# Kernel tuning notes

Hardware: AMD Instinct MI355X
Metric: run time of the kernel (lower is better)

## Reference

```python
import jax, jax.numpy as jnp
import numpy as np

B, SEQ, D = 2, 1024, 768
E, H = 8, 3072          # num_experts, expert hidden (mlp_ratio=4)
CAPACITY = 2            # k = CAPACITY * num_tokens


def setup_inputs() -> dict:
    key = jax.random.key(0)
    ks = jax.random.split(key, 6)
    x = jax.random.normal(ks[0], (B, SEQ, D), dtype=jnp.float32)
    gate_weight = jax.random.normal(ks[1], (E, D), dtype=jnp.float32) * 0.006
    w1 = jax.random.normal(ks[2], (E, D, H), dtype=jnp.float32) * (1.0 / np.sqrt(D))
    b1 = jnp.zeros((E, H), dtype=jnp.float32)
    w2 = jax.random.normal(ks[3], (E, H, D), dtype=jnp.float32) * (1.0 / np.sqrt(H))
    b2 = jnp.zeros((E, D), dtype=jnp.float32)
    return {"x": x, "gate_weight": gate_weight, "w1": w1, "b1": b1, "w2": w2, "b2": b2}


def reference(x, gate_weight, w1, b1, w2, b2):
    Bb, s, d = x.shape
    xf = x.reshape(-1, d)                     # [S, D]
    S = xf.shape[0]
    k = S * CAPACITY
    logits = xf @ gate_weight.T               # [S, E]
    scores = jax.nn.softmax(logits, axis=-1).T  # [E, S]
    # flattened top-k over all (expert, token) pairs -> sparse gate matrix
    vals, idx = jax.lax.top_k(scores.reshape(-1), k)
    gate = jnp.zeros((E * S,), dtype=x.dtype).at[idx].add(vals).reshape(E, S)
    # expert MLPs (GELU-tanh) applied per expert; zero gate entries kill
    # non-routed (expert, token) pairs -> same math as gather/MLP/scatter.
    h = jax.nn.gelu(jnp.einsum('sd,edh->esh', xf, w1) + b1[:, None, :], approximate=True)
    out = jnp.einsum('esh,ehd->esd', h, w2) + b2[:, None, :]   # [E, S, D]
    y = jnp.einsum('es,esd->sd', gate, out)    # weighted combine + sum over experts
    return y.reshape(Bb, s, d)
```

## Files before the change

kernel.cpp:

```cpp
#include <hip/hip_runtime.h>
#include <math.h>

#define S_TOK 2048
#define NEXP  8
#define DDIM  768
#define HDIM  3072
#define KSEL  4096

typedef __attribute__((ext_vector_type(8))) short short8;
typedef __attribute__((ext_vector_type(4))) float f32x4;
typedef __attribute__((ext_vector_type(2))) unsigned int u32x2;

__device__ __forceinline__ unsigned short f2bf(float f) {
  unsigned u = __float_as_uint(f);
  u += 0x7fffu + ((u >> 16) & 1u);
  return (unsigned short)(u >> 16);
}

__device__ __forceinline__ float gelu_fast(float v) {
  float u = 0.7978845608028654f * (v + 0.044715f * v * v * v);
  float t = __expf(-2.0f * fabsf(u));
  float th = (1.0f - t) / (1.0f + t);
  th = copysignf(th, u);
  return 0.5f * v * (1.0f + th);
}

__global__ __launch_bounds__(256) void zero_kernel(float* __restrict__ p, int n) {
  int i = blockIdx.x * 256 + threadIdx.x;
  if (i < n) p[i] = 0.f;
}

__global__ __launch_bounds__(256) void convx_kernel(const float* __restrict__ x,
                                                    short* __restrict__ xb) {
  int i = (blockIdx.x * 256 + threadIdx.x) * 8;
  float4 a = *(const float4*)(x + i);
  float4 b = *(const float4*)(x + i + 4);
  short8 v;
  v[0] = (short)f2bf(a.x); v[1] = (short)f2bf(a.y);
  v[2] = (short)f2bf(a.z); v[3] = (short)f2bf(a.w);
  v[4] = (short)f2bf(b.x); v[5] = (short)f2bf(b.y);
  v[6] = (short)f2bf(b.z); v[7] = (short)f2bf(b.w);
  *(short8*)(xb + i) = v;
}

__global__ __launch_bounds__(256) void gate_kernel(
    const float* __restrict__ x, const float* __restrict__ gw,
    float* __restrict__ scores)
{
  int tid  = threadIdx.x;
  int lane = tid & 63;
  int wid  = tid >> 6;
  int token = blockIdx.x * 4 + wid;
  const float* xr = x + (size_t)token * DDIM;

  float acc[NEXP];
#pragma unroll
  for (int e = 0; e < NEXP; ++e) acc[e] = 0.f;

  for (int d = lane; d < DDIM; d += 64) {
    float xv = xr[d];
#pragma unroll
    for (int e = 0; e < NEXP; ++e) acc[e] += xv * gw[e * DDIM + d];
  }
#pragma unroll
  for (int e = 0; e < NEXP; ++e) {
    for (int off = 32; off; off >>= 1) acc[e] += __shfl_down(acc[e], off, 64);
  }
  if (lane == 0) {
    float m = acc[0];
#pragma unroll
    for (int e = 1; e < NEXP; ++e) m = fmaxf(m, acc[e]);
    float p[NEXP], s = 0.f;
#pragma unroll
    for (int e = 0; e < NEXP; ++e) { p[e] = expf(acc[e] - m); s += p[e]; }
    float inv = 1.0f / s;
#pragma unroll
    for (int e = 0; e < NEXP; ++e) scores[e * S_TOK + token] = p[e] * inv;
  }
}

__device__ unsigned block_scan_excl(unsigned v, volatile unsigned* wsum) {
  int tid = threadIdx.x, lane = tid & 63, wid = tid >> 6;
  __syncthreads();
  unsigned x = v;
#pragma unroll
  for (int off = 1; off < 64; off <<= 1) {
    unsigned t = __shfl_up(x, off, 64);
    if (lane >= off) x += t;
  }
  if (lane == 63) wsum[wid] = x;
  __syncthreads();
  if (tid < 64) {
    unsigned w = (lane < 16) ? wsum[lane] : 0u;
#pragma unroll
    for (int off = 1; off < 16; off <<= 1) {
      unsigned t = __shfl_up(w, off, 64);
      if (lane >= off) w += t;
    }
    if (lane < 16) wsum[lane] = w;
  }
  __syncthreads();
  unsigned woff = (wid > 0) ? wsum[wid - 1] : 0u;
  return woff + (x - v);
}

__global__ __launch_bounds__(1024) void select_kernel(
    const float* __restrict__ scores,
    int* __restrict__ tokenlist, float* __restrict__ slotgate,
    int* __restrict__ offsets)
{
  __shared__ unsigned cnt;
  __shared__ unsigned wsum[16];
  int tid = threadIdx.x;
  int base = tid * 16;

  float sv[16]; unsigned key[16];
#pragma unroll
  for (int j = 0; j < 16; ++j) {
    sv[j] = scores[base + j];
    key[j] = __float_as_uint(sv[j]);
  }

  unsigned lo = 0, hi = 0x3F800000u;
  while (lo < hi) {
    unsigned mid = lo + ((hi - lo + 1) >> 1);
    if (tid == 0) cnt = 0;
    __syncthreads();
    unsigned c = 0;
#pragma unroll
    for (int j = 0; j < 16; ++j) c += (key[j] >= mid) ? 1u : 0u;
    for (int off = 32; off; off >>= 1) c += __shfl_down(c, off, 64);
    if ((tid & 63) == 0) atomicAdd(&cnt, c);
    __syncthreads();
    unsigned tot = cnt;
    __syncthreads();
    if (tot >= (unsigned)KSEL) lo = mid; else hi = mid - 1;
  }
  unsigned V = lo;

  if (tid == 0) cnt = 0;
  __syncthreads();
  {
    unsigned c = 0;
#pragma unroll
    for (int j = 0; j < 16; ++j) c += (key[j] > V) ? 1u : 0u;
    for (int off = 32; off; off >>= 1) c += __shfl_down(c, off, 64);
    if ((tid & 63) == 0) atomicAdd(&cnt, c);
  }
  __syncthreads();
  int need = KSEL - (int)cnt;
  __syncthreads();

  unsigned tloc = 0;
#pragma unroll
  for (int j = 0; j < 16; ++j) tloc += (key[j] == V) ? 1u : 0u;
  unsigned texcl = block_scan_excl(tloc, wsum);

  unsigned selmask = 0, sloc = 0, trun = texcl;
#pragma unroll
  for (int j = 0; j < 16; ++j) {
    bool f;
    if (key[j] > V) f = true;
    else if (key[j] == V) { f = ((int)trun < need); ++trun; }
    else f = false;
    if (f) { selmask |= (1u << j); ++sloc; }
  }
  unsigned sexcl = block_scan_excl(sloc, wsum);

  if ((tid & 127) == 0) offsets[tid >> 7] = (int)sexcl;
  if (tid == 0) offsets[NEXP] = KSEL;

  unsigned p = sexcl;
#pragma unroll
  for (int j = 0; j < 16; ++j) {
    int i = base + j;
    if (selmask & (1u << j)) {
      tokenlist[p] = i & (S_TOK - 1);
      slotgate[p] = sv[j];
      ++p;
    }
  }
}

template <int MODE>
__global__ __launch_bounds__(128) void moe_mfma(
    const short* __restrict__ Abase, const float* __restrict__ W,
    const float* __restrict__ bias, void* __restrict__ outp,
    const int* __restrict__ offsets, const int* __restrict__ tokenlist,
    const float* __restrict__ slotgate)
{
  const int e = (int)blockIdx.x;
  const int K = (MODE == 1) ? DDIM : HDIM;
  const int N = (MODE == 1) ? HDIM : DDIM;
  const int tile  = (MODE == 1) ? (int)blockIdx.z : ((int)blockIdx.z >> 2);
  const int split = (MODE == 1) ? 0 : ((int)blockIdx.z & 3);
  const int klen  = 768;
  const int kb = split * klen;

  const int r0 = offsets[e];
  const int rows = offsets[e + 1] - r0;
  const int rowbase = tile << 7;
  if (rowbase >= rows) return;
  int vr = rows - rowbase; if (vr > 128) vr = 128;
  const int colbase = (int)blockIdx.y << 6;

  __shared__ short As[128 * 40];
  __shared__ __align__(16) short Bs[32 * 64];
  const unsigned bs_lds = (unsigned)(uintptr_t)&Bs[0];

  const int tid = threadIdx.x;
  const int lane = tid & 63;
  const int wid = tid >> 6;
  const int wr = wid << 6;
  const int l15 = lane & 15;
  const int lq = lane >> 4;

  const short* arow;
  {
    int cr = (tid < vr) ? tid : (vr - 1);
    if (MODE == 1) arow = Abase + (size_t)tokenlist[r0 + rowbase + cr] * DDIM;
    else           arow = Abase + (size_t)(r0 + rowbase + cr) * HDIM + kb;
  }

  const int brow = tid >> 2;
  const int bc4 = tid & 3;
  const float* wsrc = W + (size_t)e * K * N + (size_t)kb * N + colbase + bc4 * 4;
  const int bwbase = ((tid >> 4) << 9) + ((brow & 3) << 5) + (bc4 << 3);

  f32x4 acc[4][4];
#pragma unroll
  for (int i = 0; i < 4; ++i)
#pragma unroll
    for (int j = 0; j < 4; ++j) acc[i][j] = (f32x4){0.f, 0.f, 0.f, 0.f};

  short8 av[4];
  float4 bw[4];

#define LOAD_AB(KN)                                              \
  {                                                              \
    _Pragma("unroll")                                            \
    for (int m = 0; m < 4; ++m)                                  \
      av[m] = *(const short8*)(arow + (KN) + m * 8);             \
    const float* wp = wsrc + (size_t)((KN) + brow) * N;          \
    _Pragma("unroll")                                            \
    for (int q = 0; q < 4; ++q) bw[q] = *(const float4*)(wp + q * 16); \
  }

#define WRITE_LDS()                                              \
  {                                                              \
    _Pragma("unroll")                                            \
    for (int m = 0; m < 4; ++m)                                  \
      *(short8*)&As[tid * 40 + m * 8] = av[m];                   \
    _Pragma("unroll")                                            \
    for (int q = 0; q < 4; ++q) {                                \
      u32x2 pk;                                                  \
      pk[0] = (unsigned)f2bf(bw[q].x) | ((unsigned)f2bf(bw[q].y) << 16); \
      pk[1] = (unsigned)f2bf(bw[q].z) | ((unsigned)f2bf(bw[q].w) << 16); \
      *(u32x2*)((char*)Bs + bwbase + (q << 7)) = pk;             \
    }                                                            \
  }

  LOAD_AB(0);

#pragma unroll 1
  for (int k0 = 0; k0 < klen; k0 += 32) {
    __syncthreads();
    WRITE_LDS();
    __syncthreads();
    if (k0 + 32 < klen) LOAD_AB(k0 + 32);
    short8 af[4], bfr[4];
#pragma unroll
    for (int i = 0; i < 4; ++i)
      af[i] = *(const short8*)&As[(wr + i * 16 + l15) * 40 + lq * 8];
#pragma unroll
    for (int j = 0; j < 4; ++j) {
      unsigned off = bs_lds + ((unsigned)(8 * lq + j) << 7) + ((unsigned)l15 << 3);
      union { short8 s; u32x2 u[2]; } fb;
      asm volatile("ds_read_b64_tr_b16 %0, %2 offset:0\n\t"
                   "ds_read_b64_tr_b16 %1, %2 offset:512"
                   : "=&v"(fb.u[0]), "=&v"(fb.u[1]) : "v"(off));
      bfr[j] = fb.s;
    }
    asm volatile("s_waitcnt lgkmcnt(0)" ::: "memory");
    __builtin_amdgcn_sched_barrier(0);
#pragma unroll
    for (int i = 0; i < 4; ++i)
#pragma unroll
      for (int j = 0; j < 4; ++j)
        acc[i][j] = __builtin_amdgcn_mfma_f32_16x16x32_bf16(af[i], bfr[j], acc[i][j], 0, 0, 0);
  }

  if (MODE == 1) {
    short* hb = (short*)outp;
    const float* bp = bias + (size_t)e * N + colbase;
#pragma unroll
    for (int i = 0; i < 4; ++i) {
      int rb = wr + i * 16 + lq * 4;
#pragma unroll
      for (int j = 0; j < 4; ++j) {
        int col = j * 16 + l15;
        float bvv = bp[col];
#pragma unroll
        for (int p = 0; p < 4; ++p) {
          int r = rb + p;
          if (r < vr)
            hb[(size_t)(r0 + rowbase + r) * HDIM + colbase + col] =
                (short)f2bf(gelu_fast(acc[i][j][p] + bvv));
        }
      }
    }
  } else {
    float* y = (float*)outp;
    const float* bp = bias + (size_t)e * N + colbase;
#pragma unroll
    for (int i = 0; i < 4; ++i) {
      int rb = wr + i * 16 + lq * 4;
#pragma unroll
      for (int p = 0; p < 4; ++p) {
        int r = rb + p;
        if (r < vr) {
          int gi = r0 + rowbase + r;
          float g = slotgate[gi];
          float* yrow = y + (size_t)tokenlist[gi] * N + colbase;
#pragma unroll
          for (int j = 0; j < 4; ++j) {
            int col = j * 16 + l15;
            float v = acc[i][j][p] + (split == 0 ? bp[col] : 0.f);
            atomicAdd(&yrow[col], g * v);
          }
        }
      }
    }
  }
}

extern "C" void kernel_launch(void* const* d_in, const int* in_sizes, int n_in,
                              void* d_out, int out_size, void* d_ws, size_t ws_size,
                              hipStream_t stream) {
  const float* x  = (const float*)d_in[0];
  const float* gw = (const float*)d_in[1];
  const float* w1 = (const float*)d_in[2];
  const float* b1 = (const float*)d_in[3];
  const float* w2 = (const float*)d_in[4];
  const float* b2 = (const float*)d_in[5];
  float* y = (float*)d_out;

  char* ws = (char*)d_ws;
  float* scores    = (float*)(ws);
  int*   tokenlist = (int*)(ws + (64 << 10));
  float* slotgate  = (float*)(ws + (80 << 10));
  int*   offsets   = (int*)(ws + (96 << 10));
  short* xbf       = (short*)(ws + (128 << 10));
  short* hbuf      = (short*)(ws + (128 << 10) + (size_t)S_TOK * DDIM * 2);

  zero_kernel<<<(out_size + 255) / 256, 256, 0, stream>>>(y, out_size);
  convx_kernel<<<S_TOK * DDIM / 2048, 256, 0, stream>>>(x, xbf);
  gate_kernel<<<S_TOK / 4, 256, 0, stream>>>(x, gw, scores);
  select_kernel<<<1, 1024, 0, stream>>>(scores, tokenlist, slotgate, offsets);

  dim3 g1(NEXP, HDIM / 64, 16);
  moe_mfma<1><<<g1, 128, 0, stream>>>(xbf, w1, b1, hbuf, offsets, tokenlist, slotgate);
  dim3 g2(NEXP, DDIM / 64, 64);
  moe_mfma<2><<<g2, 128, 0, stream>>>(hbuf, w2, b2, y, offsets, tokenlist, slotgate);
}
```

Before: 238.4 us.

## Pre-convert expert weights to bf16 and stage tiles via direct global-to-LDS loads

Adds a conversion kernel that writes W1 and W2 to bf16 in the workspace, chunked along the hidden dimension when the workspace is too small. The MFMA kernels then read bf16 weights with global_load_lds straight into LDS instead of loading fp32 into registers, converting and storing. The tile grows to 128x128 with 256 threads and four waves in a 2x2 layout. This removes the in-loop conversion and register staging and halves weight bytes in the GEMM loop, at the cost of extra full-weight conversion passes (read fp32, write bf16) on every call.

```diff
diff --git a/kernel.cpp b/kernel.cpp
--- a/kernel.cpp
+++ b/kernel.cpp
@@ -10,6 +10,11 @@
 typedef __attribute__((ext_vector_type(8))) short short8;
 typedef __attribute__((ext_vector_type(4))) float f32x4;
 typedef __attribute__((ext_vector_type(2))) unsigned int u32x2;
+
+#define GLOAD_LDS(GP, LP)                                            \
+  __builtin_amdgcn_global_load_lds(                                  \
+      (__attribute__((address_space(1))) void*)(GP),                 \
+      (__attribute__((address_space(3))) void*)(LP), 16, 0, 0)
 
 __device__ __forceinline__ unsigned short f2bf(float f) {
   unsigned u = __float_as_uint(f);
@@ -43,6 +48,26 @@
   *(short8*)(xb + i) = v;
 }
 
+__global__ __launch_bounds__(256) void convw_kernel(
+    const float* __restrict__ src, short* __restrict__ dst,
+    int ncols_src, int col0, int ncols_dst, int row0, int nrows, int nrows_src)
+{
+  long long i = ((long long)blockIdx.x * 256 + threadIdx.x) * 8;
+  int n = (int)(i % ncols_dst);
+  long long rr = i / ncols_dst;
+  int r = (int)(rr % nrows);
+  int e = (int)(rr / nrows);
+  const float* s = src + ((size_t)e * nrows_src + row0 + r) * ncols_src + col0 + n;
+  float4 a = *(const float4*)(s);
+  float4 b = *(const float4*)(s + 4);
+  short8 v;
+  v[0] = (short)f2bf(a.x); v[1] = (short)f2bf(a.y);
+  v[2] = (short)f2bf(a.z); v[3] = (short)f2bf(a.w);
+  v[4] = (short)f2bf(b.x); v[5] = (short)f2bf(b.y);
+  v[6] = (short)f2bf(b.z); v[7] = (short)f2bf(b.w);
+  *(short8*)(dst + i) = v;
+}
+
 __global__ __launch_bounds__(256) void gate_kernel(
     const float* __restrict__ x, const float* __restrict__ gw,
     float* __restrict__ scores)
@@ -183,49 +208,66 @@
 }
 
 template <int MODE>
-__global__ __launch_bounds__(128) void moe_mfma(
-    const short* __restrict__ Abase, const float* __restrict__ W,
+__global__ __launch_bounds__(256) void moe_mfma(
+    const short* __restrict__ Abase, const short* __restrict__ Wbf,
     const float* __restrict__ bias, void* __restrict__ outp,
     const int* __restrict__ offsets, const int* __restrict__ tokenlist,
-    const float* __restrict__ slotgate)
+    const float* __restrict__ slotgate,
+    int N, int SA, int estride, int split_bits, int cbias, int bias_en)
 {
   const int e = (int)blockIdx.x;
-  const int K = (MODE == 1) ? DDIM : HDIM;
-  const int N = (MODE == 1) ? HDIM : DDIM;
-  const int tile  = (MODE == 1) ? (int)blockIdx.z : ((int)blockIdx.z >> 2);
-  const int split = (MODE == 1) ? 0 : ((int)blockIdx.z & 3);
-  const int klen  = 768;
-  const int kb = split * klen;
+  const int tile  = (int)blockIdx.z >> split_bits;
+  const int split = (int)blockIdx.z & ((1 << split_bits) - 1);
+  const int kb = split * 768;
 
   const int r0 = offsets[e];
   const int rows = offsets[e + 1] - r0;
   const int rowbase = tile << 7;
   if (rowbase >= rows) return;
   int vr = rows - rowbase; if (vr > 128) vr = 128;
-  const int colbase = (int)blockIdx.y << 6;
-
-  __shared__ short As[128 * 40];
-  __shared__ __align__(16) short Bs[32 * 64];
+  const int colbase = (int)blockIdx.y << 7;
+
+  __shared__ __align__(16) short As[128 * 32];
+  __shared__ __align__(16) short Bs[64 * 64];
   const unsigned bs_lds = (unsigned)(uintptr_t)&Bs[0];
 
   const int tid = threadIdx.x;
   const int lane = tid & 63;
   const int wid = tid >> 6;
-  const int wr = wid << 6;
+  const int wr = (wid >> 1) << 6;
+  const int wc = (wid & 1) << 6;
   const int l15 = lane & 15;
   const int lq = lane >> 4;
 
-  const short* arow;
-  {
-    int cr = (tid < vr) ? tid : (vr - 1);
-    if (MODE == 1) arow = Abase + (size_t)tokenlist[r0 + rowbase + cr] * DDIM;
-    else           arow = Abase + (size_t)(r0 + rowbase + cr) * HDIM + kb;
-  }
-
-  const int brow = tid >> 2;
-  const int bc4 = tid & 3;
-  const float* wsrc = W + (size_t)e * K * N + (size_t)kb * N + colbase + bc4 * 4;
-  const int bwbase = ((tid >> 4) << 9) + ((brow & 3) << 5) + (bc4 << 3);
+  const int row0 = (wid * 2) * 16 + (lane >> 2);
+  const int row1 = row0 + 16;
+  const int cr0 = (row0 < vr) ? row0 : (vr - 1);
+  const int cr1 = (row1 < vr) ? row1 : (vr - 1);
+  const short *aptr0, *aptr1;
+  if (MODE == 1) {
+    aptr0 = Abase + (size_t)tokenlist[r0 + rowbase + cr0] * SA + ((lane & 3) << 3);
+    aptr1 = Abase + (size_t)tokenlist[r0 + rowbase + cr1] * SA + ((lane & 3) << 3);
+  } else {
+    aptr0 = Abase + (size_t)(r0 + rowbase + cr0) * SA + kb + ((lane & 3) << 3);
+    aptr1 = Abase + (size_t)(r0 + rowbase + cr1) * SA + kb + ((lane & 3) << 3);
+  }
+
+  const short* wb = Wbf + (size_t)e * estride + colbase +
+                    ((lane >> 3) << 4) + ((lane & 1) << 3) +
+                    (size_t)(kb + ((lane & 7) >> 1)) * N;
+  const short* bptr0 = wb + (size_t)(wid * 2 + 0) * 4 * N;
+  const short* bptr1 = wb + (size_t)(wid * 2 + 1) * 4 * N;
+
+  const int dst0 = wid * 1024;
+  const int dst1 = wid * 1024 + 512;
+
+#define STAGE(K0)                                                 \
+  {                                                               \
+    GLOAD_LDS(aptr0 + (K0), As + dst0);                           \
+    GLOAD_LDS(aptr1 + (K0), As + dst1);                           \
+    GLOAD_LDS(bptr0 + (size_t)(K0) * N, Bs + dst0);               \
+    GLOAD_LDS(bptr1 + (size_t)(K0) * N, Bs + dst1);               \
+  }
 
   f32x4 acc[4][4];
 #pragma unroll
@@ -233,56 +275,29 @@
 #pragma unroll
     for (int j = 0; j < 4; ++j) acc[i][j] = (f32x4){0.f, 0.f, 0.f, 0.f};
 
-  short8 av[4];
-  float4 bw[4];
-
-#define LOAD_AB(KN)                                              \
-  {                                                              \
-    _Pragma("unroll")                                            \
-    for (int m = 0; m < 4; ++m)                                  \
-      av[m] = *(const short8*)(arow + (KN) + m * 8);             \
-    const float* wp = wsrc + (size_t)((KN) + brow) * N;          \
-    _Pragma("unroll")                                            \
-    for (int q = 0; q < 4; ++q) bw[q] = *(const float4*)(wp + q * 16); \
-  }
-
-#define WRITE_LDS()                                              \
-  {                                                              \
-    _Pragma("unroll")                                            \
-    for (int m = 0; m < 4; ++m)                                  \
-      *(short8*)&As[tid * 40 + m * 8] = av[m];                   \
-    _Pragma("unroll")                                            \
-    for (int q = 0; q < 4; ++q) {                                \
-      u32x2 pk;                                                  \
-      pk[0] = (unsigned)f2bf(bw[q].x) | ((unsigned)f2bf(bw[q].y) << 16); \
-      pk[1] = (unsigned)f2bf(bw[q].z) | ((unsigned)f2bf(bw[q].w) << 16); \
-      *(u32x2*)((char*)Bs + bwbase + (q << 7)) = pk;             \
-    }                                                            \
-  }
-
-  LOAD_AB(0);
+  STAGE(0);
 
 #pragma unroll 1
-  for (int k0 = 0; k0 < klen; k0 += 32) {
+  for (int k0 = 0; k0 < 768; k0 += 32) {
     __syncthreads();
-    WRITE_LDS();
-    __syncthreads();
-    if (k0 + 32 < klen) LOAD_AB(k0 + 32);
     short8 af[4], bfr[4];
 #pragma unroll
     for (int i = 0; i < 4; ++i)
-      af[i] = *(const short8*)&As[(wr + i * 16 + l15) * 40 + lq * 8];
+      af[i] = *(const short8*)&As[(wr + i * 16 + l15) * 32 + lq * 8];
 #pragma unroll
     for (int j = 0; j < 4; ++j) {
-      unsigned off = bs_lds + ((unsigned)(8 * lq + j) << 7) + ((unsigned)l15 << 3);
+      unsigned off = bs_lds + ((unsigned)((lq << 4) + (wc >> 4) + j) << 7) +
+                     ((unsigned)l15 << 3);
       union { short8 s; u32x2 u[2]; } fb;
       asm volatile("ds_read_b64_tr_b16 %0, %2 offset:0\n\t"
-                   "ds_read_b64_tr_b16 %1, %2 offset:512"
+                   "ds_read_b64_tr_b16 %1, %2 offset:1024"
                    : "=&v"(fb.u[0]), "=&v"(fb.u[1]) : "v"(off));
       bfr[j] = fb.s;
     }
     asm volatile("s_waitcnt lgkmcnt(0)" ::: "memory");
     __builtin_amdgcn_sched_barrier(0);
+    __syncthreads();
+    if (k0 + 32 < 768) STAGE(k0 + 32);
 #pragma unroll
     for (int i = 0; i < 4; ++i)
 #pragma unroll
@@ -292,26 +307,27 @@
 
   if (MODE == 1) {
     short* hb = (short*)outp;
-    const float* bp = bias + (size_t)e * N + colbase;
+    const float* bp = bias + (size_t)e * HDIM + cbias + colbase;
 #pragma unroll
     for (int i = 0; i < 4; ++i) {
       int rb = wr + i * 16 + lq * 4;
 #pragma unroll
       for (int j = 0; j < 4; ++j) {
-        int col = j * 16 + l15;
+        int col = wc + j * 16 + l15;
         float bvv = bp[col];
 #pragma unroll
         for (int p = 0; p < 4; ++p) {
           int r = rb + p;
           if (r < vr)
-            hb[(size_t)(r0 + rowbase + r) * HDIM + colbase + col] =
+            hb[(size_t)(r0 + rowbase + r) * N + colbase + col] =
                 (short)f2bf(gelu_fast(acc[i][j][p] + bvv));
         }
       }
     }
   } else {
     float* y = (float*)outp;
-    const float* bp = bias + (size_t)e * N + colbase;
+    const float* bp = bias + (size_t)e * DDIM + colbase;
+    const int addb = (bias_en && split == 0);
 #pragma unroll
     for (int i = 0; i < 4; ++i) {
       int rb = wr + i * 16 + lq * 4;
@@ -321,17 +337,18 @@
         if (r < vr) {
           int gi = r0 + rowbase + r;
           float g = slotgate[gi];
-          float* yrow = y + (size_t)tokenlist[gi] * N + colbase;
+          float* yrow = y + (size_t)tokenlist[gi] * DDIM + colbase;
 #pragma unroll
           for (int j = 0; j < 4; ++j) {
-            int col = j * 16 + l15;
-            float v = acc[i][j][p] + (split == 0 ? bp[col] : 0.f);
+            int col = wc + j * 16 + l15;
+            float v = acc[i][j][p] + (addb ? bp[col] : 0.f);
             atomicAdd(&yrow[col], g * v);
           }
         }
       }
     }
   }
+#undef STAGE
 }
 
 extern "C" void kernel_launch(void* const* d_in, const int* in_sizes, int n_in,
@@ -351,15 +368,34 @@
   float* slotgate  = (float*)(ws + (80 << 10));
   int*   offsets   = (int*)(ws + (96 << 10));
   short* xbf       = (short*)(ws + (128 << 10));
-  short* hbuf      = (short*)(ws + (128 << 10) + (size_t)S_TOK * DDIM * 2);
+
+  const size_t head = (size_t)(128 << 10) + (size_t)S_TOK * DDIM * 2;
+  int nchunk = 2;
+  {
+    size_t need1 = head + (size_t)NEXP * DDIM * HDIM * 2 + (size_t)KSEL * HDIM * 2;
+    if (ws_size >= need1) nchunk = 1;
+  }
+  const int NC = HDIM / nchunk;
+  short* wbf  = (short*)(ws + head);
+  short* hbuf = wbf + (size_t)NEXP * DDIM * NC;
+  const int estride = DDIM * NC;
+  const int sb2 = (NC == 3072) ? 2 : 1;
 
   zero_kernel<<<(out_size + 255) / 256, 256, 0, stream>>>(y, out_size);
   convx_kernel<<<S_TOK * DDIM / 2048, 256, 0, stream>>>(x, xbf);
   gate_kernel<<<S_TOK / 4, 256, 0, stream>>>(x, gw, scores);
   select_kernel<<<1, 1024, 0, stream>>>(scores, tokenlist, slotgate, offsets);
 
-  dim3 g1(NEXP, HDIM / 64, 16);
-  moe_mfma<1><<<g1, 128, 0, stream>>>(xbf, w1, b1, hbuf, offsets, tokenlist, slotgate);
-  dim3 g2(NEXP, DDIM / 64, 64);
-  moe_mfma<2><<<g2, 128, 0, stream>>>(hbuf, w2, b2, y, offsets, tokenlist, slotgate);
-}
+  for (int c = 0; c < nchunk; ++c) {
+    convw_kernel<<<(NEXP * DDIM * NC) / 2048, 256, 0, stream>>>(
+        w1, wbf, HDIM, c * NC, NC, 0, DDIM, DDIM);
+    dim3 g1(NEXP, NC / 128, 16);
+    moe_mfma<1><<<g1, 256, 0, stream>>>(xbf, wbf, b1, hbuf, offsets, tokenlist,
+                                        slotgate, NC, DDIM, estride, 0, c * NC, 1);
+    convw_kernel<<<(NEXP * NC * DDIM) / 2048, 256, 0, stream>>>(
+        w2, wbf, DDIM, 0, DDIM, c * NC, NC, HDIM);
+    dim3 g2(NEXP, DDIM / 128, 16 << sb2);
+    moe_mfma<2><<<g2, 256, 0, stream>>>(hbuf, wbf, b2, y, offsets, tokenlist,
+                                        slotgate, DDIM, NC, estride, sb2, 0, c == 0);
+  }
+}
```

Result: faster. 230.6 us (-3.3%).
